# Kernel optimization log

Hardware: AMD Instinct MI355X
Metric: run time of the kernel (lower is better)

## Reference

```python
import jax, jax.numpy as jnp
import numpy as np

N = 4096        # number_of_users
IN = 1000       # in_size (items)
H1, H2 = 2048, 1024
EMB = 512
HEADS = 8
OUT = 1000


def setup_inputs() -> dict:
    key = jax.random.key(0)
    ks = iter(jax.random.split(key, 32))
    def lin(i, o):
        return jax.random.normal(next(ks), (i, o), jnp.float32) * (1.0 / np.sqrt(i))
    inp = {"batch": jax.random.normal(next(ks), (N, IN), jnp.float32)}
    for p in ("q", "k", "v"):
        inp[p + "_w1"] = lin(IN, H1); inp[p + "_b1"] = jnp.zeros((H1,), jnp.float32)
        inp[p + "_w2"] = lin(H1, H2); inp[p + "_b2"] = jnp.zeros((H2,), jnp.float32)
        inp[p + "_w3"] = lin(H2, EMB); inp[p + "_b3"] = jnp.zeros((EMB,), jnp.float32)
    inp["wo_w"] = lin(EMB, OUT)
    inp["wo_b"] = jnp.zeros((OUT,), jnp.float32)
    return inp


def _mlp(x, w1, b1, w2, b2, w3, b3):
    h = jax.nn.relu(x @ w1 + b1)
    h = jax.nn.relu(h @ w2 + b2)
    return h @ w3 + b3


def _split_heads(x):
    # [N, EMB] -> [HEADS, N, depth]
    return x.reshape(N, HEADS, EMB // HEADS).transpose(1, 0, 2)


def reference(batch,
              q_w1, q_b1, q_w2, q_b2, q_w3, q_b3,
              k_w1, k_b1, k_w2, k_b2, k_w3, k_b3,
              v_w1, v_b1, v_w2, v_b2, v_w3, v_b3,
              wo_w, wo_b):
    q = _mlp(batch, q_w1, q_b1, q_w2, q_b2, q_w3, q_b3)
    k = _mlp(batch, k_w1, k_b1, k_w2, k_b2, k_w3, k_b3)
    v = _mlp(batch, v_w1, v_b1, v_w2, v_b2, v_w3, v_b3)
    qh = jax.nn.relu(_split_heads(q))
    kh = jax.nn.relu(_split_heads(k))
    vh = _split_heads(v)
    depth = EMB // HEADS
    # ReLU-normalized attention (no softmax): scores / row-sum
    scores = jnp.einsum('hnd,hmd->hnm', qh, kh) / jnp.sqrt(jnp.float32(depth))
    denom = jnp.sum(scores, axis=-1, keepdims=True) + 1e-8
    weights = scores / denom
    att = jnp.einsum('hnm,hmd->hnd', weights, vh)   # [H, N, depth]
    att = att.transpose(1, 0, 2).reshape(N, EMB)
    return att @ wo_w + wo_b
```

## Files before the change

kernel.cpp:

```cpp
#include <hip/hip_runtime.h>
#include <hip/hip_bf16.h>


typedef __attribute__((ext_vector_type(4))) float f32x4;
typedef __attribute__((ext_vector_type(8))) short bf16x8;

static constexpr size_t OFF_XB   = 0;
static constexpr size_t OFF_WT1  = OFF_XB   + 8388608;
static constexpr size_t OFF_WT2  = OFF_WT1  + 12582912;
static constexpr size_t OFF_WT3  = OFF_WT2  + 12582912;
static constexpr size_t OFF_WTO  = OFF_WT3  + 3145728;
static constexpr size_t OFF_B1C  = OFF_WTO  + 1048576;
static constexpr size_t OFF_H1   = OFF_B1C  + 24576;
static constexpr size_t OFF_H2   = OFF_H1   + 50331648;
static constexpr size_t OFF_QKV  = OFF_H2   + 25165824;
static constexpr size_t OFF_MP   = OFF_QKV  + 12582912;
static constexpr size_t OFF_MF   = OFF_MP   + 4259840;
static constexpr size_t OFF_ATT  = OFF_MF   + 133120;

__device__ __forceinline__ void gload16(const __hip_bfloat16* g, __hip_bfloat16* l) {
  __builtin_amdgcn_global_load_lds(
      (const __attribute__((address_space(1))) void*)g,
      (__attribute__((address_space(3))) void*)l, 16, 0, 0);
}

__global__ void conv_pad_batch(const float* __restrict__ in, __hip_bfloat16* __restrict__ out) {
  int idx = blockIdx.x * 256 + threadIdx.x;
  int r = idx >> 10, c = idx & 1023;
  float v = (c < 1000) ? in[(size_t)r * 1000 + c] : 0.f;
  out[idx] = __float2bfloat16(v);
}

__global__ void concat3(const float* __restrict__ a, const float* __restrict__ b,
                        const float* __restrict__ c, float* __restrict__ out) {
  int i = blockIdx.x * 256 + threadIdx.x;
  if (i < 6144) {
    const float* src = (i < 2048) ? a : ((i < 4096) ? b : c);
    out[i] = src[i & 2047];
  }
}

__global__ void transpose_conv3(const float* __restrict__ s0, const float* __restrict__ s1,
                                const float* __restrict__ s2, __hip_bfloat16* __restrict__ outb,
                                size_t ostride, int K, int N, int Kpad) {
  const float* in = (blockIdx.z == 0) ? s0 : ((blockIdx.z == 1) ? s1 : s2);
  __hip_bfloat16* out = outb + (size_t)blockIdx.z * ostride;
  __shared__ float tile[32][33];
  int kb = blockIdx.x * 32, nb = blockIdx.y * 32;
  int tx = threadIdx.x, ty = threadIdx.y;
  for (int i = ty; i < 32; i += 8) {
    int k = kb + i, n = nb + tx;
    tile[i][tx] = (k < K && n < N) ? in[(size_t)k * N + n] : 0.f;
  }
  __syncthreads();
  for (int i = ty; i < 32; i += 8) {
    int n = nb + i, kp = kb + tx;
    out[(size_t)n * Kpad + kp] = __float2bfloat16(tile[tx][i]);
  }
}

__global__ __launch_bounds__(512, 2) void gemm_p(
    const __hip_bfloat16* __restrict__ A, int lda, size_t Az,
    const __hip_bfloat16* __restrict__ B, int ldb, size_t Bz,
    const float* __restrict__ bias0, const float* __restrict__ bias1,
    const float* __restrict__ bias2,
    __hip_bfloat16* __restrict__ Cout, int ldc, size_t Cz,
    int K, int relu) {
  __shared__ __hip_bfloat16 sm[4][2][8192];

  const int t = threadIdx.x;
  const int z = blockIdx.z;
  const int m0 = blockIdx.y * 256;
  const int n0 = blockIdx.x * 256;
  A += (size_t)z * Az;
  B += (size_t)z * Bz;
  const float* bias = (z == 0) ? bias0 : ((z == 1) ? bias1 : bias2);

  const int w = t >> 6, l = t & 63;
  const int wm = (w >> 2) * 128;
  const int wn = (w & 3) * 64;
  const int fr = l & 15, fq = l >> 4;

  {
  }
  const int rho = t >> 3;
  const int p_st = (t & 7) ^ (rho & 7);
  const int r_st = rho * 2 + (p_st >> 2);
  const int s_st = (p_st & 3) * 8;
  const __hip_bfloat16* srcA0 = A + (size_t)(m0 + r_st) * lda + s_st;
  const __hip_bfloat16* srcB0 = B + (size_t)(n0 + r_st) * ldb + s_st;

  const int p_ld = ((fr & 1) << 2) | fq;
  const int lane_sw = (fr >> 1) * 64 + ((p_ld ^ (fr >> 1)) << 3);
  const int wm32 = wm * 32, wn32 = wn * 32;

  f32x4 acc[8][4] = {};

  const int NT = K >> 5;

#define STAGE_P(BUF, KT) do {                                                  \
    const __hip_bfloat16* a_ = srcA0 + (size_t)(KT) * 32;                      \
    const __hip_bfloat16* b_ = srcB0 + (size_t)(KT) * 32;                      \
    __hip_bfloat16* lA_ = &sm[(BUF)][0][w * 512];                              \
    __hip_bfloat16* lB_ = &sm[(BUF)][1][w * 512];                              \
    gload16(a_, lA_);                                                          \
    gload16(a_ + (size_t)128 * lda, lA_ + 4096);                               \
    gload16(b_, lB_);                                                          \
    gload16(b_ + (size_t)128 * ldb, lB_ + 4096);                               \
  } while (0)

#define BODY_P(TT, VMSTR) do {                                                 \
    asm volatile("s_waitcnt vmcnt(" VMSTR ")" ::: "memory");                   \
    __builtin_amdgcn_s_barrier();                                              \
    __builtin_amdgcn_sched_barrier(0);                                         \
    const int t_ = (TT);                                                       \
    if (t_ + 3 < NT) { STAGE_P((t_ + 3) & 3, t_ + 3); }                        \
    const __hip_bfloat16* As_ = &sm[t_ & 3][0][0];                             \
    const __hip_bfloat16* Bs_ = &sm[t_ & 3][1][0];                             \
    bf16x8 af[8], bfv[4];                                                      \
    _Pragma("unroll")                                                          \
    for (int i = 0; i < 8; ++i)                                                \
      af[i] = *reinterpret_cast<const bf16x8*>(&As_[wm32 + i * 512 + lane_sw]);\
    _Pragma("unroll")                                                          \
    for (int j = 0; j < 4; ++j)                                                \
      bfv[j] = *reinterpret_cast<const bf16x8*>(&Bs_[wn32 + j * 512 + lane_sw]);\
    __builtin_amdgcn_s_setprio(1);                                             \
    _Pragma("unroll")                                                          \
    for (int i = 0; i < 8; ++i)                                                \
      _Pragma("unroll")                                                        \
      for (int j = 0; j < 4; ++j)                                              \
        acc[i][j] = __builtin_amdgcn_mfma_f32_16x16x32_bf16(af[i], bfv[j],     \
                                                            acc[i][j], 0, 0, 0);\
    __builtin_amdgcn_s_setprio(0);                                             \
  } while (0)

  STAGE_P(0, 0);
  STAGE_P(1, 1);
  STAGE_P(2, 2);

  for (int tt = 0; tt < NT - 2; ++tt) BODY_P(tt, "8");
  BODY_P(NT - 2, "4");
  BODY_P(NT - 1, "0");

#undef STAGE_P
#undef BODY_P

  float bv[4];
#pragma unroll
  for (int j = 0; j < 4; ++j) bv[j] = bias[n0 + wn + j * 16 + fr];
  __hip_bfloat16* C = Cout + (size_t)z * Cz;
#pragma unroll
  for (int i = 0; i < 8; ++i) {
#pragma unroll
    for (int j = 0; j < 4; ++j) {
      const int col = n0 + wn + j * 16 + fr;
#pragma unroll
      for (int r = 0; r < 4; ++r) {
        const int row = m0 + wm + i * 16 + fq * 4 + r;
        float v = acc[i][j][r] + bv[j];
        if (relu) v = fmaxf(v, 0.f);
        C[(size_t)row * ldc + col] = __float2bfloat16(v);
      }
    }
  }
}

__global__ __launch_bounds__(256) void gemm_bt(
    const __hip_bfloat16* __restrict__ A, int lda, size_t Az,
    const __hip_bfloat16* __restrict__ B, int ldb, size_t Bz,
    const float* __restrict__ bias0, const float* __restrict__ bias1,
    const float* __restrict__ bias2,
    void* __restrict__ Cout, int ldc, size_t Cz,
    int nlimit, int K, int epi) {
  __shared__ __hip_bfloat16 As[128 * 32];
  __shared__ __hip_bfloat16 Bs[128 * 32];
  const int t = threadIdx.x;
  const int z = blockIdx.z;
  const int m0 = blockIdx.y * 128;
  const int n0 = blockIdx.x * 128;
  A += (size_t)z * Az;
  B += (size_t)z * Bz;
  const float* bias = (z == 0) ? bias0 : ((z == 1) ? bias1 : bias2);
  const int w = t >> 6, l = t & 63;
  const int wm = (w >> 1) * 64, wn = (w & 1) * 64;
  const int fr = l & 15, fq = l >> 4;
  const int sr = t >> 2, sc = (t & 3) * 8;

  f32x4 acc[4][4] = {};

  const __hip_bfloat16* ga = A + (size_t)(m0 + sr) * lda + sc;
  const __hip_bfloat16* gb = B + (size_t)(n0 + sr) * ldb + sc;
  __hip_bfloat16* la = As + w * 512;
  __hip_bfloat16* lb = Bs + w * 512;

  for (int k0 = 0; k0 < K; k0 += 32) {
    gload16(ga, la);
    gload16(ga + (size_t)64 * lda, la + 2048);
    gload16(gb, lb);
    gload16(gb + (size_t)64 * ldb, lb + 2048);
    ga += 32; gb += 32;
    __syncthreads();
    bf16x8 af[4], bfr[4];
#pragma unroll
    for (int i = 0; i < 4; ++i) {
      af[i]  = *reinterpret_cast<const bf16x8*>(&As[(wm + i * 16 + fr) * 32 + fq * 8]);
      bfr[i] = *reinterpret_cast<const bf16x8*>(&Bs[(wn + i * 16 + fr) * 32 + fq * 8]);
    }
#pragma unroll
    for (int i = 0; i < 4; ++i)
#pragma unroll
      for (int j = 0; j < 4; ++j)
        acc[i][j] = __builtin_amdgcn_mfma_f32_16x16x32_bf16(af[i], bfr[j], acc[i][j], 0, 0, 0);
    __syncthreads();
  }

  const bool dorelu = (epi == 1) || (epi == 3 && z < 2);
  float bv[4];
#pragma unroll
  for (int j = 0; j < 4; ++j) {
    int col = n0 + wn + j * 16 + fr;
    bv[j] = (col < nlimit) ? bias[col] : 0.f;
  }
#pragma unroll
  for (int i = 0; i < 4; ++i) {
#pragma unroll
    for (int j = 0; j < 4; ++j) {
      int col = n0 + wn + j * 16 + fr;
#pragma unroll
      for (int r = 0; r < 4; ++r) {
        int row = m0 + wm + i * 16 + fq * 4 + r;
        float v = acc[i][j][r] + bv[j];
        if (dorelu) v = fmaxf(v, 0.f);
        if (epi == 2) {
          if (col < nlimit)
            ((float*)Cout)[(size_t)row * ldc + col] = v;
        } else {
          ((__hip_bfloat16*)Cout + (size_t)z * Cz)[(size_t)row * ldc + col] = __float2bfloat16(v);
        }
      }
    }
  }
}

__global__ __launch_bounds__(256) void kv_outer(const __hip_bfloat16* __restrict__ QKV, int ld,
                                                float* __restrict__ part) {
  __shared__ __hip_bfloat16 kt[128][64];
  __shared__ __hip_bfloat16 vt[128][64];
  const int t = threadIdx.x;
  const int n0 = blockIdx.x * 128;
  const int h = blockIdx.y;
#pragma unroll
  for (int it = 0; it < 4; ++it) {
    int r = it * 32 + (t >> 3);
    int c = (t & 7) * 8;
    const __hip_bfloat16* kr = &QKV[(size_t)(n0 + r) * ld + 512 + h * 64 + c];
    const __hip_bfloat16* vr = &QKV[(size_t)(n0 + r) * ld + 1024 + h * 64 + c];
    *reinterpret_cast<bf16x8*>(&kt[r][c]) = *reinterpret_cast<const bf16x8*>(kr);
    *reinterpret_cast<bf16x8*>(&vt[r][c]) = *reinterpret_cast<const bf16x8*>(vr);
  }
  __syncthreads();
  const int i = t >> 2, j0 = (t & 3) << 4;
  float acc[16] = {};
  float ks = 0.f;
  for (int r = 0; r < 128; ++r) {
    float kv = __bfloat162float(kt[r][i]);
    ks += kv;
#pragma unroll
    for (int jj = 0; jj < 16; ++jj)
      acc[jj] += kv * __bfloat162float(vt[r][j0 + jj]);
  }
  float* dst = part + ((size_t)blockIdx.x * 8 + h) * 4160;
#pragma unroll
  for (int jj = 0; jj < 16; ++jj) dst[i * 64 + j0 + jj] = acc[jj];
  if ((t & 3) == 0) dst[4096 + i] = ks;
}

__global__ void reduce_m(const float* __restrict__ part, float* __restrict__ Mfin) {
  int h = blockIdx.x, t = threadIdx.x;
  for (int idx = t; idx < 4160; idx += 256) {
    float s = 0.f;
    for (int c = 0; c < 32; ++c) s += part[((size_t)c * 8 + h) * 4160 + idx];
    Mfin[(size_t)h * 4160 + idx] = s;
  }
}

__global__ __launch_bounds__(256) void att_kernel(const __hip_bfloat16* __restrict__ QKV, int ld,
                                                  const float* __restrict__ Mfin,
                                                  __hip_bfloat16* __restrict__ att) {
  __shared__ float q[8][512];
  __shared__ float den[8][8];
  const int t = threadIdx.x;
  const int n0 = blockIdx.x * 8;
  for (int e = t; e < 8 * 512; e += 256) {
    int r = e >> 9, c = e & 511;
    q[r][c] = __bfloat162float(QKV[(size_t)(n0 + r) * ld + c]);
  }
  __syncthreads();
  if (t < 64) {
    int r = t >> 3, h = t & 7;
    const float* ks = Mfin + (size_t)h * 4160 + 4096;
    float s = 0.f;
    for (int i = 0; i < 64; ++i) s += q[r][h * 64 + i] * ks[i];
    den[r][h] = s * 0.125f + 1e-8f;
  }
  __syncthreads();
  for (int cc = 0; cc < 2; ++cc) {
    int j = t + cc * 256;
    int h = j >> 6, jh = j & 63;
    const float* Mc = Mfin + (size_t)h * 4160;
    float a0[8] = {};
    for (int i = 0; i < 64; ++i) {
      float m = Mc[i * 64 + jh];
#pragma unroll
      for (int r = 0; r < 8; ++r) a0[r] += q[r][h * 64 + i] * m;
    }
#pragma unroll
    for (int r = 0; r < 8; ++r)
      att[(size_t)(n0 + r) * 512 + j] = __float2bfloat16(a0[r] * 0.125f / den[r][h]);
  }
}

extern "C" void kernel_launch(void* const* d_in, const int* in_sizes, int n_in,
                              void* d_out, int out_size, void* d_ws, size_t ws_size,
                              hipStream_t stream) {
  const float* batch = (const float*)d_in[0];
  const float* w1[3] = {(const float*)d_in[1],  (const float*)d_in[7],  (const float*)d_in[13]};
  const float* b1[3] = {(const float*)d_in[2],  (const float*)d_in[8],  (const float*)d_in[14]};
  const float* w2[3] = {(const float*)d_in[3],  (const float*)d_in[9],  (const float*)d_in[15]};
  const float* b2[3] = {(const float*)d_in[4],  (const float*)d_in[10], (const float*)d_in[16]};
  const float* w3[3] = {(const float*)d_in[5],  (const float*)d_in[11], (const float*)d_in[17]};
  const float* b3[3] = {(const float*)d_in[6],  (const float*)d_in[12], (const float*)d_in[18]};
  const float* wow   = (const float*)d_in[19];
  const float* wob   = (const float*)d_in[20];

  char* ws = (char*)d_ws;
  __hip_bfloat16* XB  = (__hip_bfloat16*)(ws + OFF_XB);
  __hip_bfloat16* WT1 = (__hip_bfloat16*)(ws + OFF_WT1);
  __hip_bfloat16* WT2 = (__hip_bfloat16*)(ws + OFF_WT2);
  __hip_bfloat16* WT3 = (__hip_bfloat16*)(ws + OFF_WT3);
  __hip_bfloat16* WTO = (__hip_bfloat16*)(ws + OFF_WTO);
  float*          B1C = (float*)(ws + OFF_B1C);
  __hip_bfloat16* H1  = (__hip_bfloat16*)(ws + OFF_H1);
  __hip_bfloat16* H2  = (__hip_bfloat16*)(ws + OFF_H2);
  __hip_bfloat16* QKV = (__hip_bfloat16*)(ws + OFF_QKV);
  float*          MP  = (float*)(ws + OFF_MP);
  float*          MF  = (float*)(ws + OFF_MF);
  __hip_bfloat16* ATT = (__hip_bfloat16*)(ws + OFF_ATT);
  float*          OUT = (float*)d_out;

  conv_pad_batch<<<16384, 256, 0, stream>>>(batch, XB);
  concat3<<<24, 256, 0, stream>>>(b1[0], b1[1], b1[2], B1C);
  transpose_conv3<<<dim3(32, 64, 3), dim3(32, 8), 0, stream>>>(
      w1[0], w1[1], w1[2], WT1, (size_t)2048 * 1024, 1000, 2048, 1024);
  transpose_conv3<<<dim3(64, 32, 3), dim3(32, 8), 0, stream>>>(
      w2[0], w2[1], w2[2], WT2, (size_t)1024 * 2048, 2048, 1024, 2048);
  transpose_conv3<<<dim3(32, 16, 3), dim3(32, 8), 0, stream>>>(
      w3[0], w3[1], w3[2], WT3, (size_t)512 * 1024, 1024, 512, 1024);
  transpose_conv3<<<dim3(16, 32, 1), dim3(32, 8), 0, stream>>>(
      wow, wow, wow, WTO, 0, 512, 1000, 512);

  gemm_p<<<dim3(24, 16, 1), 512, 0, stream>>>(XB, 1024, 0, WT1, 1024, 0,
                                              B1C, B1C, B1C, H1, 6144, 0, 1024, 1);
  gemm_p<<<dim3(4, 16, 3), 512, 0, stream>>>(H1, 6144, 2048, WT2, 2048, (size_t)1024 * 2048,
                                             b2[0], b2[1], b2[2], H2, 3072, 1024, 2048, 1);
  gemm_bt<<<dim3(4, 32, 3), 256, 0, stream>>>(H2, 3072, 1024, WT3, 1024, (size_t)512 * 1024,
                                              b3[0], b3[1], b3[2], QKV, 1536, 512,
                                              512, 1024, 3);

  kv_outer<<<dim3(32, 8), 256, 0, stream>>>(QKV, 1536, MP);
  reduce_m<<<8, 256, 0, stream>>>(MP, MF);
  att_kernel<<<512, 256, 0, stream>>>(QKV, 1536, MF, ATT);

  gemm_bt<<<dim3(8, 32, 1), 256, 0, stream>>>(ATT, 512, 0, WTO, 512, 0,
                                              wob, wob, wob, OUT, 1000, 0,
                                              1000, 512, 2);

  (void)in_sizes; (void)n_in; (void)out_size; (void)ws_size;
}
```

Measured before the change: 287.2 us.

## Rewrite big GEMM as 8-wave K64 ping-pong with phased LDS reads

Replaces the 4-stage K=32 pipelined GEMM with a double-buffered K=64 kernel that splits each tile into four phases. In each phase the waves read one quadrant of A/B fragments from LDS, issue the global-to-LDS loads for the next quadrant, and run the MFMAs, with barriers between phases. The output mapping changes to a 2x2 arrangement of per-wave subtiles. The aim is to interleave memory and MFMA work more finely and halve the number of K iterations, at the cost of more barriers and fewer tiles in flight.

```diff
diff --git a/kernel.cpp b/kernel.cpp
--- a/kernel.cpp
+++ b/kernel.cpp
@@ -59,107 +59,128 @@
   }
 }
 
-__global__ __launch_bounds__(512, 2) void gemm_p(
+__global__ __launch_bounds__(512, 2) void gemm_p8(
     const __hip_bfloat16* __restrict__ A, int lda, size_t Az,
     const __hip_bfloat16* __restrict__ B, int ldb, size_t Bz,
     const float* __restrict__ bias0, const float* __restrict__ bias1,
     const float* __restrict__ bias2,
     __hip_bfloat16* __restrict__ Cout, int ldc, size_t Cz,
-    int K, int relu) {
-  __shared__ __hip_bfloat16 sm[4][2][8192];
-
+    int NT, int relu) {
+  __shared__ __hip_bfloat16 sm[2][4][8192];
   const int t = threadIdx.x;
   const int z = blockIdx.z;
-  const int m0 = blockIdx.y * 256;
-  const int n0 = blockIdx.x * 256;
+  const int m0 = blockIdx.y * 256, n0 = blockIdx.x * 256;
   A += (size_t)z * Az;
   B += (size_t)z * Bz;
   const float* bias = (z == 0) ? bias0 : ((z == 1) ? bias1 : bias2);
 
   const int w = t >> 6, l = t & 63;
-  const int wm = (w >> 2) * 128;
-  const int wn = (w & 3) * 64;
+  const int wm = w >> 2, wn = w & 3;
   const int fr = l & 15, fq = l >> 4;
 
+  const int row0 = t >> 3, row1 = row0 + 64;
+  const int c0 = (t & 7) ^ (row0 & 7);
+  const int c1 = (t & 7) ^ (row1 & 7);
+  const __hip_bfloat16* gA0a = A + (size_t)(m0 + row0) * lda + c0 * 8;
+  const __hip_bfloat16* gA0b = A + (size_t)(m0 + row1) * lda + c1 * 8;
+  const __hip_bfloat16* gA1a = gA0a + (size_t)128 * lda;
+  const __hip_bfloat16* gA1b = gA0b + (size_t)128 * lda;
+  const __hip_bfloat16* gB0a = B + (size_t)(n0 + row0) * ldb + c0 * 8;
+  const __hip_bfloat16* gB0b = B + (size_t)(n0 + row1) * ldb + c1 * 8;
+  const __hip_bfloat16* gB1a = gB0a + (size_t)128 * ldb;
+  const __hip_bfloat16* gB1b = gB0b + (size_t)128 * ldb;
+
+  const int baseA = (wm * 64 + fr) * 128;
+  const int baseB = (wn * 32 + fr) * 128;
+  const int xb0 = ((fq) ^ (fr & 7)) * 16;
+  const int xb1 = ((4 + fq) ^ (fr & 7)) * 16;
+
+  f32x4 acc[8][4] = {};
+  bf16x8 af[4][2], bfv[2][2];
+
+#define STG8(NXT, HALF, PA, PB, KT) do {                                       \
+    gload16((PA) + (size_t)(KT) * 64, &sm[NXT][HALF][w * 512]);                \
+    gload16((PB) + (size_t)(KT) * 64, &sm[NXT][HALF][w * 512 + 4096]);         \
+  } while (0)
+
+#define PH8(CUR, MG, NG, RDA, RDB, STG, WAITSTMT) do {                         \
+    const char* a_ = (const char*)&sm[CUR][MG][0];                             \
+    const char* b_ = (const char*)&sm[CUR][2 + (NG)][0];                       \
+    if (RDA) {                                                                 \
+      _Pragma("unroll") for (int i = 0; i < 4; ++i) {                          \
+        af[i][0] = *(const bf16x8*)(a_ + baseA + i * 2048 + xb0);              \
+        af[i][1] = *(const bf16x8*)(a_ + baseA + i * 2048 + xb1);              \
+      }                                                                        \
+    }                                                                          \
+    if (RDB) {                                                                 \
+      _Pragma("unroll") for (int j = 0; j < 2; ++j) {                          \
+        bfv[j][0] = *(const bf16x8*)(b_ + baseB + j * 2048 + xb0);             \
+        bfv[j][1] = *(const bf16x8*)(b_ + baseB + j * 2048 + xb1);             \
+      }                                                                        \
+    }                                                                          \
+    STG;                                                                       \
+    __builtin_amdgcn_s_barrier();                                              \
+    asm volatile("s_waitcnt lgkmcnt(0)" ::: "memory");                         \
+    __builtin_amdgcn_sched_barrier(0);                                         \
+    __builtin_amdgcn_s_setprio(1);                                             \
+    _Pragma("unroll") for (int ks = 0; ks < 2; ++ks)                           \
+      _Pragma("unroll") for (int i = 0; i < 4; ++i)                            \
+        _Pragma("unroll") for (int j = 0; j < 2; ++j)                          \
+          acc[(MG) * 4 + i][(NG) * 2 + j] =                                    \
+              __builtin_amdgcn_mfma_f32_16x16x32_bf16(                         \
+                  af[i][ks], bfv[j][ks], acc[(MG) * 4 + i][(NG) * 2 + j],      \
+                  0, 0, 0);                                                    \
+    __builtin_amdgcn_s_setprio(0);                                             \
+    WAITSTMT;                                                                  \
+    __builtin_amdgcn_s_barrier();                                              \
+  } while (0)
+
+  STG8(0, 0, gA0a, gA0b, 0);
+  STG8(0, 1, gA1a, gA1b, 0);
+  STG8(0, 2, gB0a, gB0b, 0);
+  STG8(0, 3, gB1a, gB1b, 0);
+  asm volatile("s_waitcnt vmcnt(0)" ::: "memory");
+  __builtin_amdgcn_s_barrier();
+
+  for (int T = 0; T < NT - 1; ++T) {
+    const int cur = T & 1, nxt = cur ^ 1;
+    const int kt = T + 1;
+    PH8(cur, 0, 0, 1, 1, STG8(nxt, 0, gA0a, gA0b, kt), (void)0);
+    PH8(cur, 1, 0, 1, 0, STG8(nxt, 1, gA1a, gA1b, kt),
+        asm volatile("s_waitcnt vmcnt(4)" ::: "memory"));
+    PH8(cur, 1, 1, 0, 1, STG8(nxt, 2, gB0a, gB0b, kt), (void)0);
+    PH8(cur, 0, 1, 1, 0, STG8(nxt, 3, gB1a, gB1b, kt),
+        asm volatile("s_waitcnt vmcnt(2)" ::: "memory"));
+  }
   {
-  }
-  const int rho = t >> 3;
-  const int p_st = (t & 7) ^ (rho & 7);
-  const int r_st = rho * 2 + (p_st >> 2);
-  const int s_st = (p_st & 3) * 8;
-  const __hip_bfloat16* srcA0 = A + (size_t)(m0 + r_st) * lda + s_st;
-  const __hip_bfloat16* srcB0 = B + (size_t)(n0 + r_st) * ldb + s_st;
-
-  const int p_ld = ((fr & 1) << 2) | fq;
-  const int lane_sw = (fr >> 1) * 64 + ((p_ld ^ (fr >> 1)) << 3);
-  const int wm32 = wm * 32, wn32 = wn * 32;
-
-  f32x4 acc[8][4] = {};
-
-  const int NT = K >> 5;
-
-#define STAGE_P(BUF, KT) do {                                                  \
-    const __hip_bfloat16* a_ = srcA0 + (size_t)(KT) * 32;                      \
-    const __hip_bfloat16* b_ = srcB0 + (size_t)(KT) * 32;                      \
-    __hip_bfloat16* lA_ = &sm[(BUF)][0][w * 512];                              \
-    __hip_bfloat16* lB_ = &sm[(BUF)][1][w * 512];                              \
-    gload16(a_, lA_);                                                          \
-    gload16(a_ + (size_t)128 * lda, lA_ + 4096);                               \
-    gload16(b_, lB_);                                                          \
-    gload16(b_ + (size_t)128 * ldb, lB_ + 4096);                               \
-  } while (0)
-
-#define BODY_P(TT, VMSTR) do {                                                 \
-    asm volatile("s_waitcnt vmcnt(" VMSTR ")" ::: "memory");                   \
-    __builtin_amdgcn_s_barrier();                                              \
-    __builtin_amdgcn_sched_barrier(0);                                         \
-    const int t_ = (TT);                                                       \
-    if (t_ + 3 < NT) { STAGE_P((t_ + 3) & 3, t_ + 3); }                        \
-    const __hip_bfloat16* As_ = &sm[t_ & 3][0][0];                             \
-    const __hip_bfloat16* Bs_ = &sm[t_ & 3][1][0];                             \
-    bf16x8 af[8], bfv[4];                                                      \
-    _Pragma("unroll")                                                          \
-    for (int i = 0; i < 8; ++i)                                                \
-      af[i] = *reinterpret_cast<const bf16x8*>(&As_[wm32 + i * 512 + lane_sw]);\
-    _Pragma("unroll")                                                          \
-    for (int j = 0; j < 4; ++j)                                                \
-      bfv[j] = *reinterpret_cast<const bf16x8*>(&Bs_[wn32 + j * 512 + lane_sw]);\
-    __builtin_amdgcn_s_setprio(1);                                             \
-    _Pragma("unroll")                                                          \
-    for (int i = 0; i < 8; ++i)                                                \
-      _Pragma("unroll")                                                        \
-      for (int j = 0; j < 4; ++j)                                              \
-        acc[i][j] = __builtin_amdgcn_mfma_f32_16x16x32_bf16(af[i], bfv[j],     \
-                                                            acc[i][j], 0, 0, 0);\
-    __builtin_amdgcn_s_setprio(0);                                             \
-  } while (0)
-
-  STAGE_P(0, 0);
-  STAGE_P(1, 1);
-  STAGE_P(2, 2);
-
-  for (int tt = 0; tt < NT - 2; ++tt) BODY_P(tt, "8");
-  BODY_P(NT - 2, "4");
-  BODY_P(NT - 1, "0");
-
-#undef STAGE_P
-#undef BODY_P
-
+    const int cur = (NT - 1) & 1;
+    PH8(cur, 0, 0, 1, 1, (void)0, (void)0);
+    PH8(cur, 1, 0, 1, 0, (void)0,
+        asm volatile("s_waitcnt vmcnt(0)" ::: "memory"));
+    PH8(cur, 1, 1, 0, 1, (void)0, (void)0);
+    PH8(cur, 0, 1, 1, 0, (void)0, (void)0);
+  }
+#undef PH8
+#undef STG8
+
+  __hip_bfloat16* C = Cout + (size_t)z * Cz;
   float bv[4];
 #pragma unroll
-  for (int j = 0; j < 4; ++j) bv[j] = bias[n0 + wn + j * 16 + fr];
-  __hip_bfloat16* C = Cout + (size_t)z * Cz;
-#pragma unroll
-  for (int i = 0; i < 8; ++i) {
-#pragma unroll
-    for (int j = 0; j < 4; ++j) {
-      const int col = n0 + wn + j * 16 + fr;
-#pragma unroll
-      for (int r = 0; r < 4; ++r) {
-        const int row = m0 + wm + i * 16 + fq * 4 + r;
-        float v = acc[i][j][r] + bv[j];
+  for (int nj = 0; nj < 4; ++nj) {
+    const int col = n0 + (nj >> 1) * 128 + wn * 32 + (nj & 1) * 16 + fr;
+    bv[nj] = bias[col];
+  }
+#pragma unroll
+  for (int mi = 0; mi < 8; ++mi) {
+    const int rowb = m0 + (mi >> 2) * 128 + wm * 64 + (mi & 3) * 16 + fq * 4;
+#pragma unroll
+    for (int nj = 0; nj < 4; ++nj) {
+      const int col = n0 + (nj >> 1) * 128 + wn * 32 + (nj & 1) * 16 + fr;
+#pragma unroll
+      for (int rr = 0; rr < 4; ++rr) {
+        float v = acc[mi][nj][rr] + bv[nj];
         if (relu) v = fmaxf(v, 0.f);
-        C[(size_t)row * ldc + col] = __float2bfloat16(v);
+        C[(size_t)(rowb + rr) * ldc + col] = __float2bfloat16(v);
       }
     }
   }
@@ -359,10 +380,10 @@
   transpose_conv3<<<dim3(16, 32, 1), dim3(32, 8), 0, stream>>>(
       wow, wow, wow, WTO, 0, 512, 1000, 512);
 
-  gemm_p<<<dim3(24, 16, 1), 512, 0, stream>>>(XB, 1024, 0, WT1, 1024, 0,
-                                              B1C, B1C, B1C, H1, 6144, 0, 1024, 1);
-  gemm_p<<<dim3(4, 16, 3), 512, 0, stream>>>(H1, 6144, 2048, WT2, 2048, (size_t)1024 * 2048,
-                                             b2[0], b2[1], b2[2], H2, 3072, 1024, 2048, 1);
+  gemm_p8<<<dim3(24, 16, 1), 512, 0, stream>>>(XB, 1024, 0, WT1, 1024, 0,
+                                               B1C, B1C, B1C, H1, 6144, 0, 16, 1);
+  gemm_p8<<<dim3(4, 16, 3), 512, 0, stream>>>(H1, 6144, 2048, WT2, 2048, (size_t)1024 * 2048,
+                                              b2[0], b2[1], b2[2], H2, 3072, 1024, 32, 1);
   gemm_bt<<<dim3(4, 32, 3), 256, 0, stream>>>(H2, 3072, 1024, WT3, 1024, (size_t)512 * 1024,
                                               b3[0], b3[1], b3[2], QKV, 1536, 512,
                                               512, 1024, 3);
```

Measured after the change: 282.7 us. Within noise of the previous version (-1.6%).
